# Optimization experiments

Measured on AMD Instinct MI355X. Metric: run time of the kernel, lower is better.

The kernel has to match this reference:

```python
import jax, jax.numpy as jnp
import numpy as np

N = 65536      # flattened tokens
K = 8192       # codebook_size
D = 64         # codebook_dim
DECAY = 0.9
EPS = 1e-05


def setup_inputs() -> dict:
    key = jax.random.key(0)
    k1, k2, k3, k4 = jax.random.split(key, 4)
    z = jax.random.normal(k1, (N, D), dtype=jnp.float32)
    # codebook initialized uniform(-1, 1) in the torch module
    weight = jax.random.uniform(k2, (K, D), dtype=jnp.float32, minval=-1.0, maxval=1.0)
    # EMA state: positive cluster sizes, embed_avg near the codebook
    cluster_size = jax.random.uniform(k3, (K,), dtype=jnp.float32)
    embed_avg = weight + 0.01 * jax.random.normal(k4, (K, D), dtype=jnp.float32)
    return {"z": z, "weight": weight, "cluster_size": cluster_size, "embed_avg": embed_avg}


def reference(z, weight, cluster_size, embed_avg):
    # VectorQuantizer.ema_update: distances -> argmin -> gather -> EMA stats -> weight refresh
    zd = jax.lax.stop_gradient(z)  # torch uses z.detach() for distance/quant_error
    # distance[n,k] = ||z_n||^2 + ||c_k||^2 - 2 z_n . c_k   (addmm pattern)
    dist = (zd * zd).sum(1, keepdims=True) + (weight * weight).sum(1) - 2.0 * (zd @ weight.T)  # [N, K]
    token = jnp.argmin(dist, axis=1)                      # [N]
    embed = weight[token]                                  # gather [N, D]
    quant_error = jnp.mean(((embed - zd) ** 2).sum(1))

    # onehot_probs.sum(0) == per-code counts; onehot.T @ z == segment sum of z
    counts = jax.ops.segment_sum(jnp.ones((zd.shape[0],), zd.dtype), token, num_segments=K)  # [K]
    embed_sum = jax.ops.segment_sum(z, token, num_segments=K)                                # [K, D]

    new_cluster_size = cluster_size * DECAY + (1.0 - DECAY) * counts
    new_embed_avg = embed_avg * DECAY + (1.0 - DECAY) * embed_sum

    # ema_weight_update with num_tokens = codebook_size
    n = new_cluster_size.sum()
    smoothed = (new_cluster_size + EPS) / (n + K * EPS) * n
    new_weight = new_embed_avg / smoothed[:, None]

    return quant_error, new_weight, new_cluster_size, new_embed_avg
```

## Files before the change

kernel.cpp:

```cpp
#include <hip/hip_runtime.h>
#include <type_traits>

#define N_TOK 65536
#define K_CODE 8192
#define D_DIM 64

constexpr float DECAY = 0.9f;
constexpr float OMD = 0.1f;
constexpr float EPS = 1e-5f;

constexpr int OUT_QE = 0;
constexpr int OUT_W  = 1;
constexpr int OUT_CS = 1 + K_CODE * D_DIM;
constexpr int OUT_EA = OUT_CS + K_CODE;

constexpr int WS_QE     = 0;
constexpr int WS_NSUM   = 1;
constexpr int WS_COUNTS = 16;
constexpr int WS_EMBSUM = WS_COUNTS + K_CODE;
constexpr int WS_CNORM  = WS_EMBSUM + K_CODE * D_DIM;
constexpr int WS_WHI    = WS_CNORM + K_CODE;
constexpr int WS_WLO    = WS_WHI + K_CODE * D_DIM / 2;
constexpr int WS_ZERO   = WS_CNORM;

typedef __attribute__((ext_vector_type(16))) float floatx16;
typedef __attribute__((ext_vector_type(8)))  short short8;
typedef __attribute__((ext_vector_type(8)))  __bf16 bf16x8;

template <typename T, typename = void> struct mfma_takes : std::false_type {};
template <typename T>
struct mfma_takes<T, std::void_t<decltype(__builtin_amdgcn_mfma_f32_32x32x16_bf16(
    std::declval<T>(), std::declval<T>(), std::declval<floatx16>(), 0, 0, 0))>>
    : std::true_type {};

__device__ __forceinline__ floatx16 MFMA(short8 a, short8 b, floatx16 c) {
  if constexpr (mfma_takes<bf16x8>::value) {
    return __builtin_amdgcn_mfma_f32_32x32x16_bf16(
        __builtin_bit_cast(bf16x8, a), __builtin_bit_cast(bf16x8, b), c, 0, 0, 0);
  } else {
    return __builtin_amdgcn_mfma_f32_32x32x16_bf16(a, b, c, 0, 0, 0);
  }
}

__device__ __forceinline__ unsigned short bf16rne(float x) {
  unsigned int u = __float_as_uint(x);
  return (unsigned short)((u + 0x7FFFu + ((u >> 16) & 1u)) >> 16);
}

__device__ __forceinline__ void gload_lds16(const unsigned short* g, unsigned short* l) {
#if defined(__has_builtin) && __has_builtin(__builtin_amdgcn_global_load_lds)
  typedef __attribute__((address_space(1))) void gvoid;
  typedef __attribute__((address_space(3))) void lvoid;
  __builtin_amdgcn_global_load_lds((gvoid*)g, (lvoid*)l, 16, 0, 0);
#else
  *(uint4*)l = *(const uint4*)g;
#endif
}

__global__ void vq_prep(const float* __restrict__ w, float* __restrict__ ws) {
  const int tid = threadIdx.x;
  const int d = tid & 63;
  const int k = blockIdx.x * 4 + (tid >> 6);
  const float v = w[(size_t)k * D_DIM + d];
  const unsigned short h = bf16rne(v);
  const float hf = __uint_as_float((unsigned int)h << 16);
  const unsigned short l = bf16rne(v - hf);
  unsigned short* whi = (unsigned short*)(ws + WS_WHI);
  unsigned short* wlo = (unsigned short*)(ws + WS_WLO);
  const int pos = k * D_DIM + (((d >> 3) ^ (k & 7)) * 8) + (d & 7);
  whi[pos] = h;
  wlo[pos] = l;
  float s = v * v;
#pragma unroll
  for (int m = 32; m >= 1; m >>= 1) s += __shfl_xor(s, m);
  if (d == 0) ws[WS_CNORM + k] = s + 64.0f;
}

__global__ __launch_bounds__(256, 2) void vq_argmin(
    const float* __restrict__ z, float* __restrict__ ws)
{
  __shared__ __align__(16) unsigned short Wbuf[2][2][2][64 * 64];
  __shared__ float mind_s[2][128];
  __shared__ int   tok_s[2][128];

  const int tid  = threadIdx.x;
  const int w    = tid >> 6;
  const int lane = tid & 63;
  const int m    = lane & 31;
  const int h    = lane >> 5;
  const int tg   = w & 1;
  const int hw   = w >> 1;
  const int tb   = blockIdx.x * 128;

  const unsigned short* whi = (const unsigned short*)(ws + WS_WHI);
  const unsigned short* wlo = (const unsigned short*)(ws + WS_WLO);
  const float* cnorm_g = ws + WS_CNORM;

  short8 ah[2][4], al[2][4];
  float znorm[2];
#pragma unroll
  for (int set = 0; set < 2; ++set) {
    const float* zrow = z + (size_t)(tb + tg * 64 + set * 32 + m) * D_DIM + 8 * h;
    float zn = 0.f;
#pragma unroll
    for (int s4 = 0; s4 < 4; ++s4) {
      const float4 v0 = *(const float4*)(zrow + 16 * s4);
      const float4 v1 = *(const float4*)(zrow + 16 * s4 + 4);
      const float vals[8] = {v0.x, v0.y, v0.z, v0.w, v1.x, v1.y, v1.z, v1.w};
#pragma unroll
      for (int j = 0; j < 8; ++j) {
        const float x = vals[j];
        zn += x * x;
        const unsigned short hb = bf16rne(x);
        const float hf = __uint_as_float((unsigned int)hb << 16);
        const unsigned short lb = bf16rne(x - hf);
        ah[set][s4][j] = (short)hb;
        al[set][s4][j] = (short)lb;
      }
    }
    zn += __shfl_xor(zn, 32);
    znorm[set] = zn;
  }

  float kmin[2][16];
#pragma unroll
  for (int set = 0; set < 2; ++set)
#pragma unroll
    for (int r = 0; r < 16; ++r) kmin[set][r] = 3.4e38f;

  const unsigned short* gplane = ((w & 1) ? wlo : whi) + (size_t)hw * 4096 * D_DIM + lane * 8;
  unsigned short* lplane = &Wbuf[hw][0][w & 1][0];
  auto issueStage = [&](int s, int b) {
    const unsigned short* src = gplane + (size_t)s * (64 * D_DIM);
    unsigned short* dst = lplane + b * (2 * 64 * 64);
#pragma unroll
    for (int i = 0; i < 8; ++i)
      gload_lds16(src + i * 512, dst + i * 512);
  };

  int xoff[4];
#pragma unroll
  for (int s4 = 0; s4 < 4; ++s4) xoff[s4] = ((2 * s4 + h) ^ (m & 7)) * 8;
  const int mrow = m * 64;

  issueStage(0, 0);
  __syncthreads();

  const floatx16 kZero = {};

  for (int s = 0; s < 64; ++s) {
    const int b = s & 1;
    if (s + 1 < 64) issueStage(s + 1, b ^ 1);

    const unsigned short* bhb = &Wbuf[hw][b][0][0];
    const unsigned short* blb = &Wbuf[hw][b][1][0];
    float cn[2];
    cn[0] = cnorm_g[hw * 4096 + s * 64 + m];
    cn[1] = cnorm_g[hw * 4096 + s * 64 + 32 + m];

#pragma unroll
    for (int j = 0; j < 2; ++j) {
      short8 bh[4], bl[4];
#pragma unroll
      for (int s4 = 0; s4 < 4; ++s4) {
        const int off = j * (32 * 64) + mrow + xoff[s4];
        bh[s4] = *(const short8*)(bhb + off);
        bl[s4] = *(const short8*)(blb + off);
      }
      floatx16 a0, a1;
      a0 = MFMA(ah[0][0], bh[0], kZero);
      a1 = MFMA(ah[1][0], bh[0], kZero);
#pragma unroll
      for (int s4 = 1; s4 < 4; ++s4) {
        a0 = MFMA(ah[0][s4], bh[s4], a0);
        a1 = MFMA(ah[1][s4], bh[s4], a1);
      }
#pragma unroll
      for (int s4 = 0; s4 < 4; ++s4) {
        a0 = MFMA(al[0][s4], bh[s4], a0);
        a1 = MFMA(al[1][s4], bh[s4], a1);
      }
#pragma unroll
      for (int s4 = 0; s4 < 4; ++s4) {
        a0 = MFMA(ah[0][s4], bl[s4], a0);
        a1 = MFMA(ah[1][s4], bl[s4], a1);
      }

      const unsigned int q = (unsigned int)(s * 2 + j);
#pragma unroll
      for (int r = 0; r < 16; ++r) {
        const float d0 = __builtin_fmaf(-2.f, a0[r], cn[j]);
        const float d1 = __builtin_fmaf(-2.f, a1[r], cn[j]);
        kmin[0][r] = fminf(kmin[0][r],
            __uint_as_float((__float_as_uint(d0) & 0xFFFFFF00u) | q));
        kmin[1][r] = fminf(kmin[1][r],
            __uint_as_float((__float_as_uint(d1) & 0xFFFFFF00u) | q));
      }
    }
    __syncthreads();
  }

#pragma unroll
  for (int set = 0; set < 2; ++set) {
#pragma unroll
    for (int r = 0; r < 16; ++r) {
      float kv = kmin[set][r];
      int mo = m;
#pragma unroll
      for (int mm = 1; mm < 32; mm <<= 1) {
        const float ov = __shfl_xor(kv, mm);
        const int   om = __shfl_xor(mo, mm);
        if (ov < kv || (ov == kv && om < mo)) { kv = ov; mo = om; }
      }
      const int mr = (r & 3) + 8 * (r >> 2) + 4 * h;
      if (m == mr) {
        const unsigned int kb = __float_as_uint(kv);
        tok_s[hw][tg * 64 + set * 32 + mr] = hw * 4096 + (int)(kb & 0xFFu) * 32 + mo;
        mind_s[hw][tg * 64 + set * 32 + mr] =
            __uint_as_float(kb & 0xFFFFFF00u) - 64.0f + znorm[set];
      }
    }
  }
  __syncthreads();

  float* counts = ws + WS_COUNTS;
  float* embsum = ws + WS_EMBSUM;

  if (tid < 128) {
    const float d0 = mind_s[0][tid], d1 = mind_s[1][tid];
    const int   i0 = tok_s[0][tid],  i1 = tok_s[1][tid];
    const bool t1 = d1 < d0;
    const float dm = t1 ? d1 : d0;
    const int   im = t1 ? i1 : i0;
    tok_s[0][tid] = im;
    float qe = dm;
#pragma unroll
    for (int mm = 32; mm >= 1; mm >>= 1) qe += __shfl_xor(qe, mm);
    if ((tid & 63) == 0) atomicAdd(ws + WS_QE, qe);
    atomicAdd(&counts[im], 1.0f);
  }
  __syncthreads();

#pragma unroll 4
  for (int t = 0; t < 32; ++t) {
    const int row = w * 32 + t;
    const int tk = tok_s[0][row];
    const float zv = z[(size_t)(tb + row) * D_DIM + lane];
    atomicAdd(&embsum[(size_t)tk * D_DIM + lane], zv);
  }
}

__global__ void vq_finalize_cs(const float* __restrict__ cluster_size,
                               float* __restrict__ ws, float* __restrict__ out)
{
  const int k = blockIdx.x * 256 + threadIdx.x;
  const float ncs = cluster_size[k] * DECAY + OMD * ws[WS_COUNTS + k];
  out[OUT_CS + k] = ncs;
  float s = ncs;
#pragma unroll
  for (int m = 32; m >= 1; m >>= 1) s += __shfl_xor(s, m);
  __shared__ float part[4];
  if ((threadIdx.x & 63) == 0) part[threadIdx.x >> 6] = s;
  __syncthreads();
  if (threadIdx.x == 0) {
    atomicAdd(ws + WS_NSUM, part[0] + part[1] + part[2] + part[3]);
    if (blockIdx.x == 0) out[OUT_QE] = ws[WS_QE] * (1.0f / N_TOK);
  }
}

__global__ void vq_finalize_w(const float* __restrict__ embed_avg,
                              const float* __restrict__ ws, float* __restrict__ out)
{
  const int idx = blockIdx.x * 256 + threadIdx.x;
  const int k = idx >> 6;
  const float nea = embed_avg[idx] * DECAY + OMD * ws[WS_EMBSUM + idx];
  out[OUT_EA + idx] = nea;
  const float n = ws[WS_NSUM];
  const float ncs = out[OUT_CS + k];
  const float sm = (ncs + EPS) / (n + K_CODE * EPS) * n;
  out[OUT_W + idx] = nea / sm;
}

extern "C" void kernel_launch(void* const* d_in, const int* in_sizes, int n_in,
                              void* d_out, int out_size, void* d_ws, size_t ws_size,
                              hipStream_t stream) {
  const float* z  = (const float*)d_in[0];
  const float* w  = (const float*)d_in[1];
  const float* cs = (const float*)d_in[2];
  const float* ea = (const float*)d_in[3];
  float* out = (float*)d_out;
  float* ws  = (float*)d_ws;

  (void)hipMemsetAsync(d_ws, 0, (size_t)WS_ZERO * sizeof(float), stream);

  vq_prep<<<K_CODE / 4, 256, 0, stream>>>(w, ws);
  vq_argmin<<<N_TOK / 128, 256, 0, stream>>>(z, ws);
  vq_finalize_cs<<<K_CODE / 256, 256, 0, stream>>>(cs, ws, out);
  vq_finalize_w<<<K_CODE * D_DIM / 256, 256, 0, stream>>>(ea, ws, out);
}
```

Before: 282.2 us.

## Fold codebook norm into MFMA and split argmin across more waves

The codebook squared norm is now stored as a bf16 hi/lo pair and added through an extra MFMA with a ones vector, and z is pre-scaled by -2. The per-element fma in the epilogue goes away and the accumulator holds the distance directly. Blocks now run 512 threads, each wave handles 32 tokens with a single accumulator, and LDS stages shrink to 32 codes. This halves per-wave register pressure so more waves can be resident, at the cost of more barriers per block and one extra MFMA per stage.

```diff
diff --git a/kernel.cpp b/kernel.cpp
--- a/kernel.cpp
+++ b/kernel.cpp
@@ -18,10 +18,10 @@
 constexpr int WS_NSUM   = 1;
 constexpr int WS_COUNTS = 16;
 constexpr int WS_EMBSUM = WS_COUNTS + K_CODE;
-constexpr int WS_CNORM  = WS_EMBSUM + K_CODE * D_DIM;
-constexpr int WS_WHI    = WS_CNORM + K_CODE;
+constexpr int WS_WHI    = WS_EMBSUM + K_CODE * D_DIM;
 constexpr int WS_WLO    = WS_WHI + K_CODE * D_DIM / 2;
-constexpr int WS_ZERO   = WS_CNORM;
+constexpr int WS_CNP    = WS_WLO + K_CODE * D_DIM / 2;
+constexpr int WS_ZERO   = WS_WHI;
 
 typedef __attribute__((ext_vector_type(16))) float floatx16;
 typedef __attribute__((ext_vector_type(8)))  short short8;
@@ -73,13 +73,19 @@
   float s = v * v;
 #pragma unroll
   for (int m = 32; m >= 1; m >>= 1) s += __shfl_xor(s, m);
-  if (d == 0) ws[WS_CNORM + k] = s + 64.0f;
-}
-
-__global__ __launch_bounds__(256, 2) void vq_argmin(
+  if (d == 0) {
+    const float cn64 = s + 64.0f;
+    const unsigned short ch = bf16rne(cn64);
+    const float chf = __uint_as_float((unsigned int)ch << 16);
+    const unsigned short cl = bf16rne(cn64 - chf);
+    ((unsigned int*)(ws + WS_CNP))[k] = (unsigned int)ch | ((unsigned int)cl << 16);
+  }
+}
+
+__global__ __launch_bounds__(512, 4) void vq_argmin(
     const float* __restrict__ z, float* __restrict__ ws)
 {
-  __shared__ __align__(16) unsigned short Wbuf[2][2][2][64 * 64];
+  __shared__ __align__(16) unsigned short Wbuf[2][2][2][32 * 64];
   __shared__ float mind_s[2][128];
   __shared__ int   tok_s[2][128];
 
@@ -88,20 +94,18 @@
   const int lane = tid & 63;
   const int m    = lane & 31;
   const int h    = lane >> 5;
-  const int tg   = w & 1;
-  const int hw   = w >> 1;
+  const int tg   = w & 3;
+  const int hw   = w >> 2;
   const int tb   = blockIdx.x * 128;
 
   const unsigned short* whi = (const unsigned short*)(ws + WS_WHI);
   const unsigned short* wlo = (const unsigned short*)(ws + WS_WLO);
-  const float* cnorm_g = ws + WS_CNORM;
-
-  short8 ah[2][4], al[2][4];
-  float znorm[2];
-#pragma unroll
-  for (int set = 0; set < 2; ++set) {
-    const float* zrow = z + (size_t)(tb + tg * 64 + set * 32 + m) * D_DIM + 8 * h;
-    float zn = 0.f;
+  const unsigned int*   cnp = (const unsigned int*)(ws + WS_CNP);
+
+  short8 ah[4], al[4];
+  float znorm = 0.f;
+  {
+    const float* zrow = z + (size_t)(tb + tg * 32 + m) * D_DIM + 8 * h;
 #pragma unroll
     for (int s4 = 0; s4 < 4; ++s4) {
       const float4 v0 = *(const float4*)(zrow + 16 * s4);
@@ -110,32 +114,39 @@
 #pragma unroll
       for (int j = 0; j < 8; ++j) {
         const float x = vals[j];
-        zn += x * x;
-        const unsigned short hb = bf16rne(x);
+        znorm += x * x;
+        const float y = -2.0f * x;
+        const unsigned short hb = bf16rne(y);
         const float hf = __uint_as_float((unsigned int)hb << 16);
-        const unsigned short lb = bf16rne(x - hf);
-        ah[set][s4][j] = (short)hb;
-        al[set][s4][j] = (short)lb;
+        const unsigned short lb = bf16rne(y - hf);
+        ah[s4][j] = (short)hb;
+        al[s4][j] = (short)lb;
       }
     }
-    zn += __shfl_xor(zn, 32);
-    znorm[set] = zn;
-  }
-
-  float kmin[2][16];
-#pragma unroll
-  for (int set = 0; set < 2; ++set)
-#pragma unroll
-    for (int r = 0; r < 16; ++r) kmin[set][r] = 3.4e38f;
-
-  const unsigned short* gplane = ((w & 1) ? wlo : whi) + (size_t)hw * 4096 * D_DIM + lane * 8;
-  unsigned short* lplane = &Wbuf[hw][0][w & 1][0];
+    znorm += __shfl_xor(znorm, 32);
+  }
+
+  short8 acn;
+  {
+    uint4 ab = {0u, 0u, 0u, 0u};
+    ab.x = (h == 0) ? 0x3F803F80u : 0u;
+    acn = __builtin_bit_cast(short8, ab);
+  }
+
+  float kmin[16];
+#pragma unroll
+  for (int r = 0; r < 16; ++r) kmin[r] = 3.4e38f;
+
   auto issueStage = [&](int s, int b) {
-    const unsigned short* src = gplane + (size_t)s * (64 * D_DIM);
-    unsigned short* dst = lplane + b * (2 * 64 * 64);
-#pragma unroll
-    for (int i = 0; i < 8; ++i)
-      gload_lds16(src + i * 512, dst + i * 512);
+#pragma unroll
+    for (int i = 0; i < 2; ++i) {
+      const int t = w * 2 + i;
+      const int half = t >> 3, plane = (t >> 2) & 1, seg = t & 3;
+      const unsigned short* src = (plane ? wlo : whi)
+          + ((size_t)half * 4096 + (size_t)s * 32) * D_DIM + seg * 512 + lane * 8;
+      unsigned short* dst = &Wbuf[half][b][plane][seg * 512];
+      gload_lds16(src, dst);
+    }
   };
 
   int xoff[4];
@@ -148,77 +159,56 @@
 
   const floatx16 kZero = {};
 
-  for (int s = 0; s < 64; ++s) {
+  for (int s = 0; s < 128; ++s) {
     const int b = s & 1;
-    if (s + 1 < 64) issueStage(s + 1, b ^ 1);
-
-    const unsigned short* bhb = &Wbuf[hw][b][0][0];
-    const unsigned short* blb = &Wbuf[hw][b][1][0];
-    float cn[2];
-    cn[0] = cnorm_g[hw * 4096 + s * 64 + m];
-    cn[1] = cnorm_g[hw * 4096 + s * 64 + 32 + m];
-
-#pragma unroll
-    for (int j = 0; j < 2; ++j) {
-      short8 bh[4], bl[4];
-#pragma unroll
-      for (int s4 = 0; s4 < 4; ++s4) {
-        const int off = j * (32 * 64) + mrow + xoff[s4];
-        bh[s4] = *(const short8*)(bhb + off);
-        bl[s4] = *(const short8*)(blb + off);
-      }
-      floatx16 a0, a1;
-      a0 = MFMA(ah[0][0], bh[0], kZero);
-      a1 = MFMA(ah[1][0], bh[0], kZero);
-#pragma unroll
-      for (int s4 = 1; s4 < 4; ++s4) {
-        a0 = MFMA(ah[0][s4], bh[s4], a0);
-        a1 = MFMA(ah[1][s4], bh[s4], a1);
-      }
-#pragma unroll
-      for (int s4 = 0; s4 < 4; ++s4) {
-        a0 = MFMA(al[0][s4], bh[s4], a0);
-        a1 = MFMA(al[1][s4], bh[s4], a1);
-      }
-#pragma unroll
-      for (int s4 = 0; s4 < 4; ++s4) {
-        a0 = MFMA(ah[0][s4], bl[s4], a0);
-        a1 = MFMA(ah[1][s4], bl[s4], a1);
-      }
-
-      const unsigned int q = (unsigned int)(s * 2 + j);
-#pragma unroll
-      for (int r = 0; r < 16; ++r) {
-        const float d0 = __builtin_fmaf(-2.f, a0[r], cn[j]);
-        const float d1 = __builtin_fmaf(-2.f, a1[r], cn[j]);
-        kmin[0][r] = fminf(kmin[0][r],
-            __uint_as_float((__float_as_uint(d0) & 0xFFFFFF00u) | q));
-        kmin[1][r] = fminf(kmin[1][r],
-            __uint_as_float((__float_as_uint(d1) & 0xFFFFFF00u) | q));
-      }
+    const unsigned int cnq = cnp[hw * 4096 + s * 32 + m];
+    if (s + 1 < 128) issueStage(s + 1, b ^ 1);
+
+    short8 bh[4], bl[4];
+#pragma unroll
+    for (int s4 = 0; s4 < 4; ++s4) {
+      bh[s4] = *(const short8*)&Wbuf[hw][b][0][mrow + xoff[s4]];
+      bl[s4] = *(const short8*)&Wbuf[hw][b][1][mrow + xoff[s4]];
+    }
+    short8 bcn;
+    {
+      uint4 bb = {0u, 0u, 0u, 0u};
+      bb.x = (h == 0) ? cnq : 0u;
+      bcn = __builtin_bit_cast(short8, bb);
+    }
+
+    floatx16 acc = MFMA(acn, bcn, kZero);
+#pragma unroll
+    for (int s4 = 0; s4 < 4; ++s4) acc = MFMA(ah[s4], bh[s4], acc);
+#pragma unroll
+    for (int s4 = 0; s4 < 4; ++s4) acc = MFMA(al[s4], bh[s4], acc);
+#pragma unroll
+    for (int s4 = 0; s4 < 4; ++s4) acc = MFMA(ah[s4], bl[s4], acc);
+
+#pragma unroll
+    for (int r = 0; r < 16; ++r) {
+      kmin[r] = fminf(kmin[r],
+          __uint_as_float((__float_as_uint(acc[r]) & 0xFFFFFF00u) | (unsigned)s));
     }
     __syncthreads();
   }
 
 #pragma unroll
-  for (int set = 0; set < 2; ++set) {
-#pragma unroll
-    for (int r = 0; r < 16; ++r) {
-      float kv = kmin[set][r];
-      int mo = m;
-#pragma unroll
-      for (int mm = 1; mm < 32; mm <<= 1) {
-        const float ov = __shfl_xor(kv, mm);
-        const int   om = __shfl_xor(mo, mm);
-        if (ov < kv || (ov == kv && om < mo)) { kv = ov; mo = om; }
-      }
-      const int mr = (r & 3) + 8 * (r >> 2) + 4 * h;
-      if (m == mr) {
-        const unsigned int kb = __float_as_uint(kv);
-        tok_s[hw][tg * 64 + set * 32 + mr] = hw * 4096 + (int)(kb & 0xFFu) * 32 + mo;
-        mind_s[hw][tg * 64 + set * 32 + mr] =
-            __uint_as_float(kb & 0xFFFFFF00u) - 64.0f + znorm[set];
-      }
+  for (int r = 0; r < 16; ++r) {
+    float kv = kmin[r];
+    int mo = m;
+#pragma unroll
+    for (int mm = 1; mm < 32; mm <<= 1) {
+      const float ov = __shfl_xor(kv, mm);
+      const int   om = __shfl_xor(mo, mm);
+      if (ov < kv || (ov == kv && om < mo)) { kv = ov; mo = om; }
+    }
+    const int mr = (r & 3) + 8 * (r >> 2) + 4 * h;
+    if (m == mr) {
+      const unsigned int kb = __float_as_uint(kv);
+      tok_s[hw][tg * 32 + mr] = hw * 4096 + (int)(kb & 0xFFu) * 32 + mo;
+      mind_s[hw][tg * 32 + mr] =
+          __uint_as_float(kb & 0xFFFFFF00u) - 64.0f + znorm;
     }
   }
   __syncthreads();
@@ -242,8 +232,8 @@
   __syncthreads();
 
 #pragma unroll 4
-  for (int t = 0; t < 32; ++t) {
-    const int row = w * 32 + t;
+  for (int t = 0; t < 16; ++t) {
+    const int row = w * 16 + t;
     const int tk = tok_s[0][row];
     const float zv = z[(size_t)(tb + row) * D_DIM + lane];
     atomicAdd(&embsum[(size_t)tk * D_DIM + lane], zv);
@@ -294,7 +284,7 @@
   (void)hipMemsetAsync(d_ws, 0, (size_t)WS_ZERO * sizeof(float), stream);
 
   vq_prep<<<K_CODE / 4, 256, 0, stream>>>(w, ws);
-  vq_argmin<<<N_TOK / 128, 256, 0, stream>>>(z, ws);
+  vq_argmin<<<N_TOK / 128, 512, 0, stream>>>(z, ws);
   vq_finalize_cs<<<K_CODE / 256, 256, 0, stream>>>(cs, ws, out);
   vq_finalize_w<<<K_CODE * D_DIM / 256, 256, 0, stream>>>(ea, ws, out);
 }
```

Measured after the change: 282.1 us. Within noise of the previous version (-0.0%).

## Give each wave a private LDS pipeline and fold codebook norm into MFMA

Applied to the files above, without the earlier changes.

Each wave now streams its own 32-code slice of the hi/lo bf16 codebook and the packed norm into private LDS double buffers. Waits use explicit waitcnt instead of block-wide __syncthreads per stage. The -2 scale is folded into the z operand, and the codebook norm (split into bf16 hi/lo) enters through an extra MFMA that seeds the accumulator, which removes the per-element FMA before the min. The cost is one extra MFMA per tile, a one-wide extra prefetch at the loop end, and reliance on hand-written vmcnt counts being right.

```diff
diff --git a/kernel.cpp b/kernel.cpp
--- a/kernel.cpp
+++ b/kernel.cpp
@@ -18,10 +18,10 @@
 constexpr int WS_NSUM   = 1;
 constexpr int WS_COUNTS = 16;
 constexpr int WS_EMBSUM = WS_COUNTS + K_CODE;
-constexpr int WS_CNORM  = WS_EMBSUM + K_CODE * D_DIM;
-constexpr int WS_WHI    = WS_CNORM + K_CODE;
+constexpr int WS_WHI    = WS_EMBSUM + K_CODE * D_DIM;
 constexpr int WS_WLO    = WS_WHI + K_CODE * D_DIM / 2;
-constexpr int WS_ZERO   = WS_CNORM;
+constexpr int WS_CNP    = WS_WLO + K_CODE * D_DIM / 2;
+constexpr int WS_ZERO   = WS_WHI;
 
 typedef __attribute__((ext_vector_type(16))) float floatx16;
 typedef __attribute__((ext_vector_type(8)))  short short8;
@@ -54,6 +54,15 @@
   __builtin_amdgcn_global_load_lds((gvoid*)g, (lvoid*)l, 16, 0, 0);
 #else
   *(uint4*)l = *(const uint4*)g;
+#endif
+}
+__device__ __forceinline__ void gload_lds4(const unsigned int* g, unsigned int* l) {
+#if defined(__has_builtin) && __has_builtin(__builtin_amdgcn_global_load_lds)
+  typedef __attribute__((address_space(1))) void gvoid;
+  typedef __attribute__((address_space(3))) void lvoid;
+  __builtin_amdgcn_global_load_lds((gvoid*)g, (lvoid*)l, 4, 0, 0);
+#else
+  *l = *g;
 #endif
 }
 
@@ -73,13 +82,20 @@
   float s = v * v;
 #pragma unroll
   for (int m = 32; m >= 1; m >>= 1) s += __shfl_xor(s, m);
-  if (d == 0) ws[WS_CNORM + k] = s + 64.0f;
+  if (d == 0) {
+    const float cn64 = s + 64.0f;
+    const unsigned short ch = bf16rne(cn64);
+    const float chf = __uint_as_float((unsigned int)ch << 16);
+    const unsigned short cl = bf16rne(cn64 - chf);
+    ((unsigned int*)(ws + WS_CNP))[k] = (unsigned int)ch | ((unsigned int)cl << 16);
+  }
 }
 
 __global__ __launch_bounds__(256, 2) void vq_argmin(
     const float* __restrict__ z, float* __restrict__ ws)
 {
-  __shared__ __align__(16) unsigned short Wbuf[2][2][2][64 * 64];
+  __shared__ __align__(16) unsigned short Wbuf[4][2][2][32 * 64];
+  __shared__ unsigned int Wcn[4][2][64];
   __shared__ float mind_s[2][128];
   __shared__ int   tok_s[2][128];
 
@@ -88,13 +104,26 @@
   const int lane = tid & 63;
   const int m    = lane & 31;
   const int h    = lane >> 5;
-  const int tg   = w & 1;
-  const int hw   = w >> 1;
+  const int hw   = w & 1;
+  const int tg   = w >> 1;
   const int tb   = blockIdx.x * 128;
 
-  const unsigned short* whi = (const unsigned short*)(ws + WS_WHI);
-  const unsigned short* wlo = (const unsigned short*)(ws + WS_WLO);
-  const float* cnorm_g = ws + WS_CNORM;
+  const unsigned short* whiP = (const unsigned short*)(ws + WS_WHI) + (size_t)hw * 4096 * D_DIM;
+  const unsigned short* wloP = (const unsigned short*)(ws + WS_WLO) + (size_t)hw * 4096 * D_DIM;
+  const unsigned int*   cnpP = (const unsigned int*)(ws + WS_CNP) + hw * 4096;
+
+  auto issueStage = [&](int s, int b) {
+    const size_t roff = (size_t)s * (32 * D_DIM) + lane * 8;
+#pragma unroll
+    for (int i = 0; i < 4; ++i)
+      gload_lds16(whiP + roff + i * 512, &Wbuf[w][b][0][i * 512]);
+#pragma unroll
+    for (int i = 0; i < 4; ++i)
+      gload_lds16(wloP + roff + i * 512, &Wbuf[w][b][1][i * 512]);
+    gload_lds4(cnpP + s * 32 + lane, &Wcn[w][b][0]);
+  };
+
+  issueStage(0, 0);
 
   short8 ah[2][4], al[2][4];
   float znorm[2];
@@ -111,9 +140,10 @@
       for (int j = 0; j < 8; ++j) {
         const float x = vals[j];
         zn += x * x;
-        const unsigned short hb = bf16rne(x);
+        const float y = -2.0f * x;
+        const unsigned short hb = bf16rne(y);
         const float hf = __uint_as_float((unsigned int)hb << 16);
-        const unsigned short lb = bf16rne(x - hf);
+        const unsigned short lb = bf16rne(y - hf);
         ah[set][s4][j] = (short)hb;
         al[set][s4][j] = (short)lb;
       }
@@ -122,82 +152,71 @@
     znorm[set] = zn;
   }
 
+  short8 acn;
+  {
+    uint4 ab = {0u, 0u, 0u, 0u};
+    ab.x = (h == 0) ? 0x3F803F80u : 0u;
+    acn = __builtin_bit_cast(short8, ab);
+  }
+
   float kmin[2][16];
 #pragma unroll
   for (int set = 0; set < 2; ++set)
 #pragma unroll
     for (int r = 0; r < 16; ++r) kmin[set][r] = 3.4e38f;
-
-  const unsigned short* gplane = ((w & 1) ? wlo : whi) + (size_t)hw * 4096 * D_DIM + lane * 8;
-  unsigned short* lplane = &Wbuf[hw][0][w & 1][0];
-  auto issueStage = [&](int s, int b) {
-    const unsigned short* src = gplane + (size_t)s * (64 * D_DIM);
-    unsigned short* dst = lplane + b * (2 * 64 * 64);
-#pragma unroll
-    for (int i = 0; i < 8; ++i)
-      gload_lds16(src + i * 512, dst + i * 512);
-  };
 
   int xoff[4];
 #pragma unroll
   for (int s4 = 0; s4 < 4; ++s4) xoff[s4] = ((2 * s4 + h) ^ (m & 7)) * 8;
   const int mrow = m * 64;
-
-  issueStage(0, 0);
-  __syncthreads();
-
   const floatx16 kZero = {};
 
-  for (int s = 0; s < 64; ++s) {
+  for (int s = 0; s < 128; ++s) {
     const int b = s & 1;
-    if (s + 1 < 64) issueStage(s + 1, b ^ 1);
-
-    const unsigned short* bhb = &Wbuf[hw][b][0][0];
-    const unsigned short* blb = &Wbuf[hw][b][1][0];
-    float cn[2];
-    cn[0] = cnorm_g[hw * 4096 + s * 64 + m];
-    cn[1] = cnorm_g[hw * 4096 + s * 64 + 32 + m];
-
-#pragma unroll
-    for (int j = 0; j < 2; ++j) {
-      short8 bh[4], bl[4];
-#pragma unroll
-      for (int s4 = 0; s4 < 4; ++s4) {
-        const int off = j * (32 * 64) + mrow + xoff[s4];
-        bh[s4] = *(const short8*)(bhb + off);
-        bl[s4] = *(const short8*)(blb + off);
-      }
-      floatx16 a0, a1;
-      a0 = MFMA(ah[0][0], bh[0], kZero);
-      a1 = MFMA(ah[1][0], bh[0], kZero);
-#pragma unroll
-      for (int s4 = 1; s4 < 4; ++s4) {
-        a0 = MFMA(ah[0][s4], bh[s4], a0);
-        a1 = MFMA(ah[1][s4], bh[s4], a1);
-      }
-#pragma unroll
-      for (int s4 = 0; s4 < 4; ++s4) {
-        a0 = MFMA(al[0][s4], bh[s4], a0);
-        a1 = MFMA(al[1][s4], bh[s4], a1);
-      }
-#pragma unroll
-      for (int s4 = 0; s4 < 4; ++s4) {
-        a0 = MFMA(ah[0][s4], bl[s4], a0);
-        a1 = MFMA(ah[1][s4], bl[s4], a1);
-      }
-
-      const unsigned int q = (unsigned int)(s * 2 + j);
-#pragma unroll
-      for (int r = 0; r < 16; ++r) {
-        const float d0 = __builtin_fmaf(-2.f, a0[r], cn[j]);
-        const float d1 = __builtin_fmaf(-2.f, a1[r], cn[j]);
-        kmin[0][r] = fminf(kmin[0][r],
-            __uint_as_float((__float_as_uint(d0) & 0xFFFFFF00u) | q));
-        kmin[1][r] = fminf(kmin[1][r],
-            __uint_as_float((__float_as_uint(d1) & 0xFFFFFF00u) | q));
-      }
-    }
-    __syncthreads();
+    asm volatile("s_waitcnt lgkmcnt(0)" ::: "memory");
+    issueStage((s + 1) & 127, b ^ 1);
+    asm volatile("s_waitcnt vmcnt(9)" ::: "memory");
+
+    short8 bh[4], bl[4];
+#pragma unroll
+    for (int s4 = 0; s4 < 4; ++s4) {
+      bh[s4] = *(const short8*)&Wbuf[w][b][0][mrow + xoff[s4]];
+      bl[s4] = *(const short8*)&Wbuf[w][b][1][mrow + xoff[s4]];
+    }
+    short8 bcn;
+    {
+      uint4 bb = {0u, 0u, 0u, 0u};
+      bb.x = (h == 0) ? Wcn[w][b][m] : 0u;
+      bcn = __builtin_bit_cast(short8, bb);
+    }
+
+    const floatx16 head = MFMA(acn, bcn, kZero);
+    floatx16 a0, a1;
+    a0 = MFMA(ah[0][0], bh[0], head);
+    a1 = MFMA(ah[1][0], bh[0], head);
+#pragma unroll
+    for (int s4 = 1; s4 < 4; ++s4) {
+      a0 = MFMA(ah[0][s4], bh[s4], a0);
+      a1 = MFMA(ah[1][s4], bh[s4], a1);
+    }
+#pragma unroll
+    for (int s4 = 0; s4 < 4; ++s4) {
+      a0 = MFMA(al[0][s4], bh[s4], a0);
+      a1 = MFMA(al[1][s4], bh[s4], a1);
+    }
+#pragma unroll
+    for (int s4 = 0; s4 < 4; ++s4) {
+      a0 = MFMA(ah[0][s4], bl[s4], a0);
+      a1 = MFMA(ah[1][s4], bl[s4], a1);
+    }
+
+#pragma unroll
+    for (int r = 0; r < 16; ++r) {
+      kmin[0][r] = fminf(kmin[0][r],
+          __uint_as_float((__float_as_uint(a0[r]) & 0xFFFFFF00u) | (unsigned)s));
+      kmin[1][r] = fminf(kmin[1][r],
+          __uint_as_float((__float_as_uint(a1[r]) & 0xFFFFFF00u) | (unsigned)s));
+    }
   }
 
 #pragma unroll
@@ -215,9 +234,9 @@
       const int mr = (r & 3) + 8 * (r >> 2) + 4 * h;
       if (m == mr) {
         const unsigned int kb = __float_as_uint(kv);
-        tok_s[hw][tg * 64 + set * 32 + mr] = hw * 4096 + (int)(kb & 0xFFu) * 32 + mo;
-        mind_s[hw][tg * 64 + set * 32 + mr] =
-            __uint_as_float(kb & 0xFFFFFF00u) - 64.0f + znorm[set];
+        const int t = tg * 64 + set * 32 + mr;
+        tok_s[hw][t] = hw * 4096 + (int)(kb & 0xFFu) * 32 + mo;
+        mind_s[hw][t] = __uint_as_float(kb & 0xFFFFFF00u) - 64.0f + znorm[set];
       }
     }
   }
```

Result: slower. 320.7 us (+13.7%).
